# Kernel optimization log

Hardware: AMD Instinct MI355X
Metric: run time of the kernel (lower is better)

The kernel has to match this reference:

```python
import jax, jax.numpy as jnp
import numpy as np

DIM = 1024
D_INNER = 2048

def setup_inputs() -> dict:
    key = jax.random.key(0)
    ks = jax.random.split(key, 8)
    B, T = 8, 1024
    x = jax.random.normal(ks[0], (B, T, DIM), dtype=jnp.float32)
    h0 = jnp.zeros((B, D_INNER), dtype=jnp.float32)
    # params (xavier-ish scales)
    in_proj_w = jax.random.normal(ks[1], (D_INNER, DIM), dtype=jnp.float32) * (2.0 / (DIM + D_INNER)) ** 0.5
    out_proj_w = jax.random.normal(ks[2], (DIM, D_INNER), dtype=jnp.float32) * (2.0 / (DIM + D_INNER)) ** 0.5
    c_h = jax.random.uniform(ks[3], (D_INNER,), jnp.float32, -0.1, 0.1)
    # spectral normalization as in _init_weights
    c_h = c_h * jnp.minimum(1.0, 0.99 / jnp.abs(jnp.fft.fft(c_h)).max())
    c_x = jax.random.uniform(ks[4], (D_INNER,), jnp.float32, -0.1, 0.1)
    c_x = c_x * jnp.minimum(1.0, 0.99 / jnp.abs(jnp.fft.fft(c_x)).max())
    b = jnp.zeros((D_INNER,), dtype=jnp.float32)
    W_gate = jax.random.normal(ks[5], (D_INNER, D_INNER), dtype=jnp.float32) * (1.0 / D_INNER) ** 0.5
    b_gate = jnp.zeros((D_INNER,), dtype=jnp.float32)
    return {"x": x, "h0": h0, "in_proj_w": in_proj_w, "out_proj_w": out_proj_w,
            "c_h": c_h, "c_x": c_x, "b": b, "W_gate": W_gate, "b_gate": b_gate}

def _circ_apply_fft(fft_c, v):
    # circ(c) @ v along last axis via real FFT; v: [..., D]
    D = v.shape[-1]
    return jnp.fft.irfft(fft_c * jnp.fft.rfft(v, axis=-1), n=D, axis=-1)

def reference(x, h0, in_proj_w, out_proj_w, c_h, c_x, b, W_gate, b_gate):
    B, T, _ = x.shape
    D = h0.shape[-1]
    x_proj = jnp.einsum('btd,ed->bte', x, in_proj_w)  # [B,T,D_inner]
    # gate path (fully parallel over T)
    gate = jax.nn.silu(jnp.einsum('bte,fe->btf', x_proj, W_gate) + b_gate)
    # input circulant contribution, parallel over all tokens
    pre = _circ_apply_fft(jnp.fft.rfft(c_x), x_proj) + b  # [B,T,D]
    fft_ch = jnp.fft.rfft(c_h)

    def step(h_prev, pre_t):
        h_new = jnp.tanh(_circ_apply_fft(fft_ch, h_prev) + pre_t)
        return h_new, h_new

    pre_tbd = jnp.transpose(pre, (1, 0, 2))  # [T,B,D]
    h_final, h_seq = jax.lax.scan(step, h0, pre_tbd)  # h_seq: [T,B,D]
    cell_out = jnp.transpose(h_seq, (1, 0, 2)) * gate  # [B,T,D]
    output = jnp.einsum('bte,de->btd', cell_out, out_proj_w)  # [B,T,dim]
    return output, h_final
```

## Files before the change

kernel.cpp:

```cpp
#include <hip/hip_runtime.h>
#include <cstdint>
#include <cstddef>

#define DI 2048
#define DM 1024
#define BB 8
#define TT 1024
#define ROWS (BB*TT)

typedef short  short8 __attribute__((ext_vector_type(8)));
typedef float  f32x4  __attribute__((ext_vector_type(4)));

__device__ __forceinline__ unsigned short f2bf(float f) {
  unsigned int u = __builtin_bit_cast(unsigned int, f);
  u = u + 0x7fffu + ((u >> 16) & 1u);
  return (unsigned short)(u >> 16);
}
__device__ __forceinline__ float fast_tanh(float x) {
  float ax = fabsf(x);
  float e  = __expf(-2.0f * ax);
  float t  = (1.0f - e) / (1.0f + e);
  return x < 0.0f ? -t : t;
}
__device__ __forceinline__ float silu_f(float z) {
  return z / (1.0f + __expf(-z));
}
__device__ __forceinline__ unsigned mulpk(unsigned a, unsigned b) {
  float a0 = __builtin_bit_cast(float, a << 16);
  float a1 = __builtin_bit_cast(float, a & 0xffff0000u);
  float b0 = __builtin_bit_cast(float, b << 16);
  float b1 = __builtin_bit_cast(float, b & 0xffff0000u);
  unsigned r0 = f2bf(a0 * b0), r1 = f2bf(a1 * b1);
  return r0 | (r1 << 16);
}
__device__ __forceinline__ uint4 pack8(const unsigned short* q) {
  uint4 p;
  p.x = (unsigned)q[0] | ((unsigned)q[1] << 16);
  p.y = (unsigned)q[2] | ((unsigned)q[3] << 16);
  p.z = (unsigned)q[4] | ((unsigned)q[5] << 16);
  p.w = (unsigned)q[6] | ((unsigned)q[7] << 16);
  return p;
}

__global__ void cast_k(const float* __restrict__ s, short* __restrict__ d, int n4) {
  int i = blockIdx.x * 256 + threadIdx.x;
  if (i >= n4) return;
  float4 f = ((const float4*)s)[i];
  unsigned lo = (unsigned)f2bf(f.x) | ((unsigned)f2bf(f.y) << 16);
  unsigned hi = (unsigned)f2bf(f.z) | ((unsigned)f2bf(f.w) << 16);
  uint2 o; o.x = lo; o.y = hi;
  ((uint2*)d)[i] = o;
}

__global__ void build_cx_k(const float* __restrict__ cx, short* __restrict__ C) {
  int tid = blockIdx.x * 256 + threadIdx.x;
  int n   = tid >> 8;
  int k0  = (tid & 255) * 8;
  unsigned short q[8];
#pragma unroll
  for (int j = 0; j < 8; ++j) q[j] = f2bf(cx[(n - (k0 + j)) & (DI - 1)]);
  *(uint4*)(C + (size_t)n * DI + k0) = pack8(q);
}

__global__ __launch_bounds__(256) void gemm_k(
    const short* __restrict__ A, const short* __restrict__ A2,
    const short* __restrict__ Bt,
    int M, int N, int K, int mode, const float* __restrict__ bias,
    float* __restrict__ outF, short* __restrict__ outH)
{
  __shared__ __align__(16) short As[128 * 40];
  __shared__ __align__(16) short Bs[128 * 40];
  const int tid  = threadIdx.x;
  const int m0   = blockIdx.y * 128, n0 = blockIdx.x * 128;
  const int wave = tid >> 6, lane = tid & 63;
  const int wy = wave >> 1, wx = wave & 1;
  const int l = lane & 15, G = lane >> 4;
  const int srow = tid >> 1, sseg = tid & 1;

  f32x4 acc[4][4];
#pragma unroll
  for (int i = 0; i < 4; ++i)
#pragma unroll
    for (int j = 0; j < 4; ++j) acc[i][j] = (f32x4){0.f, 0.f, 0.f, 0.f};

  for (int k0 = 0; k0 < K; k0 += 32) {
    if (k0) __syncthreads();
    const short* ga = A  + (size_t)(m0 + srow) * K + k0 + sseg * 16;
    const short* gb = Bt + (size_t)(n0 + srow) * K + k0 + sseg * 16;
    uint4 a0 = *(const uint4*)ga;
    uint4 a1 = *(const uint4*)(ga + 8);
    if (A2) {
      const short* g2 = A2 + (size_t)(m0 + srow) * K + k0 + sseg * 16;
      uint4 m0v = *(const uint4*)g2;
      uint4 m1v = *(const uint4*)(g2 + 8);
      a0.x = mulpk(a0.x, m0v.x); a0.y = mulpk(a0.y, m0v.y);
      a0.z = mulpk(a0.z, m0v.z); a0.w = mulpk(a0.w, m0v.w);
      a1.x = mulpk(a1.x, m1v.x); a1.y = mulpk(a1.y, m1v.y);
      a1.z = mulpk(a1.z, m1v.z); a1.w = mulpk(a1.w, m1v.w);
    }
    uint4 b0 = *(const uint4*)gb;
    uint4 b1 = *(const uint4*)(gb + 8);
    *(uint4*)&As[srow * 40 + sseg * 16]     = a0;
    *(uint4*)&As[srow * 40 + sseg * 16 + 8] = a1;
    *(uint4*)&Bs[srow * 40 + sseg * 16]     = b0;
    *(uint4*)&Bs[srow * 40 + sseg * 16 + 8] = b1;
    __syncthreads();
    short8 af[4], bfv[4];
#pragma unroll
    for (int i = 0; i < 4; ++i) af[i]  = *(const short8*)&As[(64 * wy + 16 * i + l) * 40 + 8 * G];
#pragma unroll
    for (int j = 0; j < 4; ++j) bfv[j] = *(const short8*)&Bs[(64 * wx + 16 * j + l) * 40 + 8 * G];
#pragma unroll
    for (int i = 0; i < 4; ++i)
#pragma unroll
      for (int j = 0; j < 4; ++j)
        acc[i][j] = __builtin_amdgcn_mfma_f32_16x16x32_bf16(af[i], bfv[j], acc[i][j], 0, 0, 0);
  }

#pragma unroll
  for (int j = 0; j < 4; ++j) {
    const int c = n0 + 64 * wx + 16 * j + l;
    float bv = 0.f;
    if (mode == 1 || mode == 2) bv = bias[c];
#pragma unroll
    for (int i = 0; i < 4; ++i) {
      const int r0 = m0 + 64 * wy + 16 * i + 4 * G;
#pragma unroll
      for (int v = 0; v < 4; ++v) {
        float z = acc[i][j][v] + bv;
        size_t off = (size_t)(r0 + v) * N + c;
        if (mode == 0)      outH[off] = (short)f2bf(z);
        else if (mode == 2) outH[off] = (short)f2bf(silu_f(z));
        else                outF[off] = z;
      }
    }
  }
}

__global__ __launch_bounds__(512, 2) void fused_k(
    const float* __restrict__ pre, const float* __restrict__ h0,
    const float* __restrict__ ch, short* __restrict__ hseq,
    float* __restrict__ hfin,
    const short* __restrict__ xproj, const short* __restrict__ wg,
    const float* __restrict__ bg, short* __restrict__ gate)
{
  __shared__ __align__(16) char smem[69632];
  const int bid = blockIdx.x;
  const int tid = threadIdx.x;

  if (bid < BB) {
    short* h_lds = (short*)smem;
    float* part  = (float*)(smem + 4096);
    const int b    = bid;
    const int kg   = tid >> 6;
    const int lane = tid & 63;
    const int q    = lane & 15;
    const int G    = lane >> 4;
    const float* preB = pre + (size_t)b * TT * DI;

    short8 av[22];
#pragma unroll
    for (int idx = 0; idx < 22; ++idx) {
      const int base = 16 * (idx - 14) + q - 8 * G - 256 * kg;
      short8 v;
#pragma unroll
      for (int j = 0; j < 8; ++j)
        v[j] = (short)f2bf(ch[(base - j) & (DI - 1)]);
      av[idx] = v;
    }

    {
      float4 hv = *(const float4*)(h0 + b * DI + 4 * tid);
      unsigned lo = (unsigned)f2bf(hv.x) | ((unsigned)f2bf(hv.y) << 16);
      unsigned hi = (unsigned)f2bf(hv.z) | ((unsigned)f2bf(hv.w) << 16);
      const int blk = tid >> 1;
      const int pb  = blk ^ ((blk >> 4) & 7);
      uint2 w; w.x = lo; w.y = hi;
      *(uint2*)&h_lds[pb * 8 + 4 * (tid & 1)] = w;
    }
    float4 pcur = *(const float4*)(preB + 4 * tid);
    __syncthreads();

    const int rbase = 32 * kg + G + 16 * q;

    for (int t = 0; t < TT; ++t) {
      const float* pn = preB + (size_t)(t + 1 < TT ? t + 1 : t) * DI;
      float4 pf = *(const float4*)(pn + 4 * tid);

      f32x4 acc[8];
#pragma unroll
      for (int mt = 0; mt < 8; ++mt) acc[mt] = (f32x4){0.f, 0.f, 0.f, 0.f};

#pragma unroll
      for (int s = 0; s < 8; ++s) {
        const int blk = (rbase + 4 * s) & 255;
        const int pb  = blk ^ ((blk >> 4) & 7);
        short8 bv = *(const short8*)&h_lds[pb * 8];
#pragma unroll
        for (int mt = 0; mt < 8; ++mt)
          acc[mt] = __builtin_amdgcn_mfma_f32_16x16x32_bf16(av[mt - 2 * s + 14], bv, acc[mt], 0, 0, 0);
      }

      {
        float* pk = part + (kg << 11);
#pragma unroll
        for (int mt = 0; mt < 8; ++mt) {
          const int nb  = 4 * mt + G + 32 * q;
          const int pnb = nb ^ ((nb >> 5) & 7);
          *(f32x4*)&pk[4 * pnb] = acc[mt];
        }
      }
      __syncthreads();

      {
        const int pnb = tid ^ ((tid >> 5) & 7);
        const float* pp = part + 4 * pnb;
        float4 c0 = *(const float4*)(pp);
        float4 c1 = *(const float4*)(pp + 2048);
        float4 c2 = *(const float4*)(pp + 4096);
        float4 c3 = *(const float4*)(pp + 6144);
        float4 c4 = *(const float4*)(pp + 8192);
        float4 c5 = *(const float4*)(pp + 10240);
        float4 c6 = *(const float4*)(pp + 12288);
        float4 c7 = *(const float4*)(pp + 14336);
        float z0 = ((c0.x + c1.x) + (c2.x + c3.x)) + ((c4.x + c5.x) + (c6.x + c7.x)) + pcur.x;
        float z1 = ((c0.y + c1.y) + (c2.y + c3.y)) + ((c4.y + c5.y) + (c6.y + c7.y)) + pcur.y;
        float z2 = ((c0.z + c1.z) + (c2.z + c3.z)) + ((c4.z + c5.z) + (c6.z + c7.z)) + pcur.z;
        float z3 = ((c0.w + c1.w) + (c2.w + c3.w)) + ((c4.w + c5.w) + (c6.w + c7.w)) + pcur.w;
        float t0 = fast_tanh(z0), t1 = fast_tanh(z1);
        float t2 = fast_tanh(z2), t3 = fast_tanh(z3);
        unsigned lo = (unsigned)f2bf(t0) | ((unsigned)f2bf(t1) << 16);
        unsigned hi = (unsigned)f2bf(t2) | ((unsigned)f2bf(t3) << 16);
        const int blk = tid >> 1;
        const int pb  = blk ^ ((blk >> 4) & 7);
        uint2 w; w.x = lo; w.y = hi;
        *(uint2*)&h_lds[pb * 8 + 4 * (tid & 1)] = w;
        *(uint2*)(hseq + (size_t)(b * TT + t) * DI + 4 * tid) = w;
        if (t == TT - 1) {
          float4 hf; hf.x = t0; hf.y = t1; hf.z = t2; hf.w = t3;
          *(float4*)(hfin + b * DI + 4 * tid) = hf;
        }
      }
      __syncthreads();
      pcur = pf;
    }
  } else {
    short* As = (short*)smem;
    short* Bs = (short*)(smem + 20480);
    const int wid = tid >> 6, lane = tid & 63;
    const int wy = wid >> 1, wx = wid & 1;
    const int l = lane & 15, G = lane >> 4;

    for (int tile = bid - BB; tile < 512; tile += 248) {
      const int m0 = (tile & 31) * 256, n0 = (tile >> 5) * 128;
      f32x4 acc[4][4];
#pragma unroll
      for (int i = 0; i < 4; ++i)
#pragma unroll
        for (int j = 0; j < 4; ++j) acc[i][j] = (f32x4){0.f, 0.f, 0.f, 0.f};

      for (int k0 = 0; k0 < DI; k0 += 32) {
        __syncthreads();
        const short* ga = xproj + (size_t)(m0 + (tid >> 1)) * DI + k0 + (tid & 1) * 16;
        const short* gb = wg    + (size_t)(n0 + (tid >> 2)) * DI + k0 + (tid & 3) * 8;
        uint4 a0 = *(const uint4*)ga;
        uint4 a1 = *(const uint4*)(ga + 8);
        uint4 b0 = *(const uint4*)gb;
        *(uint4*)&As[(tid >> 1) * 40 + (tid & 1) * 16]     = a0;
        *(uint4*)&As[(tid >> 1) * 40 + (tid & 1) * 16 + 8] = a1;
        *(uint4*)&Bs[(tid >> 2) * 40 + (tid & 3) * 8]      = b0;
        __syncthreads();
        short8 af[4], bfv[4];
#pragma unroll
        for (int i = 0; i < 4; ++i) af[i]  = *(const short8*)&As[(64 * wy + 16 * i + l) * 40 + 8 * G];
#pragma unroll
        for (int j = 0; j < 4; ++j) bfv[j] = *(const short8*)&Bs[(64 * wx + 16 * j + l) * 40 + 8 * G];
#pragma unroll
        for (int i = 0; i < 4; ++i)
#pragma unroll
          for (int j = 0; j < 4; ++j)
            acc[i][j] = __builtin_amdgcn_mfma_f32_16x16x32_bf16(af[i], bfv[j], acc[i][j], 0, 0, 0);
      }
#pragma unroll
      for (int j = 0; j < 4; ++j) {
        const int c = n0 + 64 * wx + 16 * j + l;
        const float bv = bg[c];
#pragma unroll
        for (int i = 0; i < 4; ++i) {
          const int r0 = m0 + 64 * wy + 16 * i + 4 * G;
#pragma unroll
          for (int v = 0; v < 4; ++v) {
            float z = acc[i][j][v] + bv;
            gate[(size_t)(r0 + v) * DI + c] = (short)f2bf(silu_f(z));
          }
        }
      }
      __syncthreads();
    }
  }
}

extern "C" void kernel_launch(void* const* d_in, const int* in_sizes, int n_in,
                              void* d_out, int out_size, void* d_ws, size_t ws_size,
                              hipStream_t stream) {
  const float* x    = (const float*)d_in[0];
  const float* h0   = (const float*)d_in[1];
  const float* win  = (const float*)d_in[2];
  const float* wout = (const float*)d_in[3];
  const float* ch   = (const float*)d_in[4];
  const float* cx   = (const float*)d_in[5];
  const float* bb   = (const float*)d_in[6];
  const float* wg   = (const float*)d_in[7];
  const float* bg   = (const float*)d_in[8];
  float* out = (float*)d_out;

  char* ws = (char*)d_ws;
  short* o_xb    = (short*)(ws + 0);
  short* o_win   = (short*)(ws + 16777216);
  short* o_cx    = (short*)(ws + 20971520);
  short* o_hseq  = (short*)(ws + 0);
  short* o_xproj = (short*)(ws + 33554432);
  float* o_pre   = (float*)(ws + 67108864);
  short* o_wout  = (short*)(ws + 67108864);
  short* o_gate  = (short*)(ws + 134217728);
  short* o_wg    = (short*)(ws + 167772160);

  cast_k<<<8192, 256, 0, stream>>>(x,   o_xb,  (BB * TT * DM) / 4);
  cast_k<<<2048, 256, 0, stream>>>(win, o_win, (DI * DM) / 4);
  cast_k<<<4096, 256, 0, stream>>>(wg,  o_wg,  (DI * DI) / 4);
  build_cx_k<<<2048, 256, 0, stream>>>(cx, o_cx);

  gemm_k<<<dim3(DI / 128, ROWS / 128), 256, 0, stream>>>(
      o_xb, nullptr, o_win, ROWS, DI, DM, 0, nullptr, nullptr, o_xproj);

  gemm_k<<<dim3(DI / 128, ROWS / 128), 256, 0, stream>>>(
      o_xproj, nullptr, o_cx, ROWS, DI, DI, 1, bb, o_pre, nullptr);

  fused_k<<<256, 512, 0, stream>>>(o_pre, h0, ch, o_hseq,
                                   out + (size_t)BB * TT * DM,
                                   o_xproj, o_wg, bg, o_gate);

  cast_k<<<2048, 256, 0, stream>>>(wout, o_wout, (DM * DI) / 4);

  gemm_k<<<dim3(DM / 128, ROWS / 128), 256, 0, stream>>>(
      o_hseq, o_gate, o_wout, ROWS, DM, DI, 3, nullptr, out, nullptr);
}
```

Baseline: 2.290 ms.

## Process two batch rows per scan block and defer hseq stores

Each scan workgroup now runs two independent batch recurrences, so only four blocks do the scan instead of eight and more blocks are free for the gate GEMM. Interleaving two independent MFMA chains per timestep is meant to hide latency within the serial step and share the circulant register fragments. The hseq global store is deferred by one step to move it off the critical path. In exchange, shared memory doubles to 136KB, which may lower occupancy for the GEMM blocks, and each scan step does twice the work, which can lengthen the serial critical path.

```diff
diff --git a/kernel.cpp b/kernel.cpp
--- a/kernel.cpp
+++ b/kernel.cpp
@@ -7,6 +7,7 @@
 #define BB 8
 #define TT 1024
 #define ROWS (BB*TT)
+#define NSCAN 4
 
 typedef short  short8 __attribute__((ext_vector_type(8)));
 typedef float  f32x4  __attribute__((ext_vector_type(4)));
@@ -144,19 +145,16 @@
     const short* __restrict__ xproj, const short* __restrict__ wg,
     const float* __restrict__ bg, short* __restrict__ gate)
 {
-  __shared__ __align__(16) char smem[69632];
+  __shared__ __align__(16) char smem[139264];
   const int bid = blockIdx.x;
   const int tid = threadIdx.x;
 
-  if (bid < BB) {
-    short* h_lds = (short*)smem;
-    float* part  = (float*)(smem + 4096);
-    const int b    = bid;
+  if (bid < NSCAN) {
+    float* part = (float*)(smem + 8192);
     const int kg   = tid >> 6;
     const int lane = tid & 63;
     const int q    = lane & 15;
     const int G    = lane >> 4;
-    const float* preB = pre + (size_t)b * TT * DI;
 
     short8 av[22];
 #pragma unroll
@@ -169,7 +167,11 @@
       av[idx] = v;
     }
 
-    {
+    float4 pcur[2];
+#pragma unroll
+    for (int bt = 0; bt < 2; ++bt) {
+      short* h_lds = (short*)(smem + bt * 4096);
+      const int b = 2 * bid + bt;
       float4 hv = *(const float4*)(h0 + b * DI + 4 * tid);
       unsigned lo = (unsigned)f2bf(hv.x) | ((unsigned)f2bf(hv.y) << 16);
       unsigned hi = (unsigned)f2bf(hv.z) | ((unsigned)f2bf(hv.w) << 16);
@@ -177,32 +179,44 @@
       const int pb  = blk ^ ((blk >> 4) & 7);
       uint2 w; w.x = lo; w.y = hi;
       *(uint2*)&h_lds[pb * 8 + 4 * (tid & 1)] = w;
-    }
-    float4 pcur = *(const float4*)(preB + 4 * tid);
+      pcur[bt] = *(const float4*)(pre + (size_t)b * TT * DI + 4 * tid);
+    }
     __syncthreads();
 
     const int rbase = 32 * kg + G + 16 * q;
+    uint2 wprev[2];
+    wprev[0] = (uint2){0u, 0u}; wprev[1] = (uint2){0u, 0u};
 
     for (int t = 0; t < TT; ++t) {
-      const float* pn = preB + (size_t)(t + 1 < TT ? t + 1 : t) * DI;
-      float4 pf = *(const float4*)(pn + 4 * tid);
-
-      f32x4 acc[8];
-#pragma unroll
-      for (int mt = 0; mt < 8; ++mt) acc[mt] = (f32x4){0.f, 0.f, 0.f, 0.f};
-
-#pragma unroll
-      for (int s = 0; s < 8; ++s) {
-        const int blk = (rbase + 4 * s) & 255;
-        const int pb  = blk ^ ((blk >> 4) & 7);
-        short8 bv = *(const short8*)&h_lds[pb * 8];
-#pragma unroll
-        for (int mt = 0; mt < 8; ++mt)
-          acc[mt] = __builtin_amdgcn_mfma_f32_16x16x32_bf16(av[mt - 2 * s + 14], bv, acc[mt], 0, 0, 0);
-      }
-
-      {
-        float* pk = part + (kg << 11);
+      float4 pf[2];
+#pragma unroll
+      for (int bt = 0; bt < 2; ++bt) {
+        const float* pn = pre + (size_t)(2 * bid + bt) * TT * DI
+                        + (size_t)(t + 1 < TT ? t + 1 : t) * DI;
+        pf[bt] = *(const float4*)(pn + 4 * tid);
+      }
+      if (t) {
+#pragma unroll
+        for (int bt = 0; bt < 2; ++bt)
+          *(uint2*)(hseq + (size_t)((2 * bid + bt) * TT + t - 1) * DI + 4 * tid) = wprev[bt];
+      }
+
+#pragma unroll
+      for (int bt = 0; bt < 2; ++bt) {
+        const short* h_lds = (const short*)(smem + bt * 4096);
+        f32x4 acc[8];
+#pragma unroll
+        for (int mt = 0; mt < 8; ++mt) acc[mt] = (f32x4){0.f, 0.f, 0.f, 0.f};
+#pragma unroll
+        for (int s = 0; s < 8; ++s) {
+          const int blk = (rbase + 4 * s) & 255;
+          const int pb  = blk ^ ((blk >> 4) & 7);
+          short8 bv = *(const short8*)&h_lds[pb * 8];
+#pragma unroll
+          for (int mt = 0; mt < 8; ++mt)
+            acc[mt] = __builtin_amdgcn_mfma_f32_16x16x32_bf16(av[mt - 2 * s + 14], bv, acc[mt], 0, 0, 0);
+        }
+        float* pk = part + bt * 16384 + (kg << 11);
 #pragma unroll
         for (int mt = 0; mt < 8; ++mt) {
           const int nb  = 4 * mt + G + 32 * q;
@@ -212,9 +226,10 @@
       }
       __syncthreads();
 
-      {
+#pragma unroll
+      for (int bt = 0; bt < 2; ++bt) {
         const int pnb = tid ^ ((tid >> 5) & 7);
-        const float* pp = part + 4 * pnb;
+        const float* pp = part + bt * 16384 + 4 * pnb;
         float4 c0 = *(const float4*)(pp);
         float4 c1 = *(const float4*)(pp + 2048);
         float4 c2 = *(const float4*)(pp + 4096);
@@ -223,10 +238,10 @@
         float4 c5 = *(const float4*)(pp + 10240);
         float4 c6 = *(const float4*)(pp + 12288);
         float4 c7 = *(const float4*)(pp + 14336);
-        float z0 = ((c0.x + c1.x) + (c2.x + c3.x)) + ((c4.x + c5.x) + (c6.x + c7.x)) + pcur.x;
-        float z1 = ((c0.y + c1.y) + (c2.y + c3.y)) + ((c4.y + c5.y) + (c6.y + c7.y)) + pcur.y;
-        float z2 = ((c0.z + c1.z) + (c2.z + c3.z)) + ((c4.z + c5.z) + (c6.z + c7.z)) + pcur.z;
-        float z3 = ((c0.w + c1.w) + (c2.w + c3.w)) + ((c4.w + c5.w) + (c6.w + c7.w)) + pcur.w;
+        float z0 = ((c0.x + c1.x) + (c2.x + c3.x)) + ((c4.x + c5.x) + (c6.x + c7.x)) + pcur[bt].x;
+        float z1 = ((c0.y + c1.y) + (c2.y + c3.y)) + ((c4.y + c5.y) + (c6.y + c7.y)) + pcur[bt].y;
+        float z2 = ((c0.z + c1.z) + (c2.z + c3.z)) + ((c4.z + c5.z) + (c6.z + c7.z)) + pcur[bt].z;
+        float z3 = ((c0.w + c1.w) + (c2.w + c3.w)) + ((c4.w + c5.w) + (c6.w + c7.w)) + pcur[bt].w;
         float t0 = fast_tanh(z0), t1 = fast_tanh(z1);
         float t2 = fast_tanh(z2), t3 = fast_tanh(z3);
         unsigned lo = (unsigned)f2bf(t0) | ((unsigned)f2bf(t1) << 16);
@@ -234,16 +249,20 @@
         const int blk = tid >> 1;
         const int pb  = blk ^ ((blk >> 4) & 7);
         uint2 w; w.x = lo; w.y = hi;
+        short* h_lds = (short*)(smem + bt * 4096);
         *(uint2*)&h_lds[pb * 8 + 4 * (tid & 1)] = w;
-        *(uint2*)(hseq + (size_t)(b * TT + t) * DI + 4 * tid) = w;
+        wprev[bt] = w;
         if (t == TT - 1) {
           float4 hf; hf.x = t0; hf.y = t1; hf.z = t2; hf.w = t3;
-          *(float4*)(hfin + b * DI + 4 * tid) = hf;
+          *(float4*)(hfin + (2 * bid + bt) * DI + 4 * tid) = hf;
         }
       }
       __syncthreads();
-      pcur = pf;
-    }
+      pcur[0] = pf[0]; pcur[1] = pf[1];
+    }
+#pragma unroll
+    for (int bt = 0; bt < 2; ++bt)
+      *(uint2*)(hseq + (size_t)((2 * bid + bt) * TT + TT - 1) * DI + 4 * tid) = wprev[bt];
   } else {
     short* As = (short*)smem;
     short* Bs = (short*)(smem + 20480);
@@ -251,7 +270,7 @@
     const int wy = wid >> 1, wx = wid & 1;
     const int l = lane & 15, G = lane >> 4;
 
-    for (int tile = bid - BB; tile < 512; tile += 248) {
+    for (int tile = bid - NSCAN; tile < 512; tile += (256 - NSCAN)) {
       const int m0 = (tile & 31) * 256, n0 = (tile >> 5) * 128;
       f32x4 acc[4][4];
 #pragma unroll
```

After: 3.780 ms. 1.65x slower.

## Use 32x32x16 MFMA with 4 scan waves and defer hseq stores

Applied to the files above, without the earlier changes.

The recurrent scan step now runs its circulant matvec on only four waves, each using 32x32x16 bf16 MFMAs with two accumulators instead of eight waves of 16x16x32 MFMAs. This halves the cross-wave partial-sum reduction through LDS from eight to four partials. The global store of each hidden state is deferred by one step so it sits off the critical path before the barrier. The cost is more registers per active wave for the circulant fragments, four idle waves during the MFMA phase, and a larger shared allocation that may reduce occupancy for the overlapped gate GEMM blocks.

```diff
diff --git a/kernel.cpp b/kernel.cpp
--- a/kernel.cpp
+++ b/kernel.cpp
@@ -7,9 +7,11 @@
 #define BB 8
 #define TT 1024
 #define ROWS (BB*TT)
+#define NSCAN 8
 
 typedef short  short8 __attribute__((ext_vector_type(8)));
 typedef float  f32x4  __attribute__((ext_vector_type(4)));
+typedef float  f32x16 __attribute__((ext_vector_type(16)));
 
 __device__ __forceinline__ unsigned short f2bf(float f) {
   unsigned int u = __builtin_bit_cast(unsigned int, f);
@@ -144,29 +146,32 @@
     const short* __restrict__ xproj, const short* __restrict__ wg,
     const float* __restrict__ bg, short* __restrict__ gate)
 {
-  __shared__ __align__(16) char smem[69632];
+  __shared__ __align__(16) char smem[81920];
   const int bid = blockIdx.x;
   const int tid = threadIdx.x;
 
-  if (bid < BB) {
+  if (bid < NSCAN) {
     short* h_lds = (short*)smem;
     float* part  = (float*)(smem + 4096);
     const int b    = bid;
-    const int kg   = tid >> 6;
+    const int wid  = tid >> 6;
     const int lane = tid & 63;
-    const int q    = lane & 15;
-    const int G    = lane >> 4;
+    const int kg   = wid;
+    const int qc   = lane & 31;
+    const int Gc   = lane >> 5;
     const float* preB = pre + (size_t)b * TT * DI;
 
-    short8 av[22];
-#pragma unroll
-    for (int idx = 0; idx < 22; ++idx) {
-      const int base = 16 * (idx - 14) + q - 8 * G - 256 * kg;
-      short8 v;
-#pragma unroll
-      for (int j = 0; j < 8; ++j)
-        v[j] = (short)f2bf(ch[(base - j) & (DI - 1)]);
-      av[idx] = v;
+    short8 av[34];
+    if (wid < 4) {
+#pragma unroll
+      for (int idx = 0; idx < 34; ++idx) {
+        const int base = 16 * (idx - 31) + qc - 8 * Gc - 512 * kg;
+        short8 v;
+#pragma unroll
+        for (int j = 0; j < 8; ++j)
+          v[j] = (short)f2bf(ch[(base - j) & (DI - 1)]);
+        av[idx] = v;
+      }
     }
 
     {
@@ -181,52 +186,60 @@
     float4 pcur = *(const float4*)(preB + 4 * tid);
     __syncthreads();
 
-    const int rbase = 32 * kg + G + 16 * q;
+    uint2 wprev; wprev.x = 0u; wprev.y = 0u;
 
     for (int t = 0; t < TT; ++t) {
       const float* pn = preB + (size_t)(t + 1 < TT ? t + 1 : t) * DI;
       float4 pf = *(const float4*)(pn + 4 * tid);
-
-      f32x4 acc[8];
-#pragma unroll
-      for (int mt = 0; mt < 8; ++mt) acc[mt] = (f32x4){0.f, 0.f, 0.f, 0.f};
-
-#pragma unroll
-      for (int s = 0; s < 8; ++s) {
-        const int blk = (rbase + 4 * s) & 255;
-        const int pb  = blk ^ ((blk >> 4) & 7);
-        short8 bv = *(const short8*)&h_lds[pb * 8];
-#pragma unroll
-        for (int mt = 0; mt < 8; ++mt)
-          acc[mt] = __builtin_amdgcn_mfma_f32_16x16x32_bf16(av[mt - 2 * s + 14], bv, acc[mt], 0, 0, 0);
-      }
+      if (t)
+        *(uint2*)(hseq + (size_t)(b * TT + t - 1) * DI + 4 * tid) = wprev;
+
+      if (wid < 4) {
+        f32x16 acc0, acc1;
+#pragma unroll
+        for (int v = 0; v < 16; ++v) { acc0[v] = 0.f; acc1[v] = 0.f; }
+#pragma unroll
+        for (int s = 0; s < 32; ++s) {
+          const int blk = (64 * kg + 2 * s + Gc + 8 * qc) & 255;
+          const int pb  = blk ^ ((blk >> 4) & 7);
+          short8 bv = *(const short8*)&h_lds[pb * 8];
+          acc0 = __builtin_amdgcn_mfma_f32_32x32x16_bf16(av[31 - s], bv, acc0, 0, 0, 0);
+          acc1 = __builtin_amdgcn_mfma_f32_32x32x16_bf16(av[33 - s], bv, acc1, 0, 0, 0);
+        }
+        float* pk = part + (kg << 11);
+#pragma unroll
+        for (int s4 = 0; s4 < 4; ++s4) {
+          {
+            const int nb  = 2 * s4 + Gc + 16 * qc;
+            const int pnb = nb ^ ((nb >> 4) & 7);
+            float4 w;
+            w.x = acc0[4 * s4 + 0]; w.y = acc0[4 * s4 + 1];
+            w.z = acc0[4 * s4 + 2]; w.w = acc0[4 * s4 + 3];
+            *(float4*)&pk[4 * pnb] = w;
+          }
+          {
+            const int nb  = 8 + 2 * s4 + Gc + 16 * qc;
+            const int pnb = nb ^ ((nb >> 4) & 7);
+            float4 w;
+            w.x = acc1[4 * s4 + 0]; w.y = acc1[4 * s4 + 1];
+            w.z = acc1[4 * s4 + 2]; w.w = acc1[4 * s4 + 3];
+            *(float4*)&pk[4 * pnb] = w;
+          }
+        }
+      }
+      __syncthreads();
 
       {
-        float* pk = part + (kg << 11);
-#pragma unroll
-        for (int mt = 0; mt < 8; ++mt) {
-          const int nb  = 4 * mt + G + 32 * q;
-          const int pnb = nb ^ ((nb >> 5) & 7);
-          *(f32x4*)&pk[4 * pnb] = acc[mt];
-        }
-      }
-      __syncthreads();
-
-      {
-        const int pnb = tid ^ ((tid >> 5) & 7);
-        const float* pp = part + 4 * pnb;
+        const int pe = tid ^ ((tid >> 4) & 7);
+        const float* pp = part + 4 * pe;
         float4 c0 = *(const float4*)(pp);
         float4 c1 = *(const float4*)(pp + 2048);
         float4 c2 = *(const float4*)(pp + 4096);
         float4 c3 = *(const float4*)(pp + 6144);
-        float4 c4 = *(const float4*)(pp + 8192);
-        float4 c5 = *(const float4*)(pp + 10240);
-        float4 c6 = *(const float4*)(pp + 12288);
-        float4 c7 = *(const float4*)(pp + 14336);
-        float z0 = ((c0.x + c1.x) + (c2.x + c3.x)) + ((c4.x + c5.x) + (c6.x + c7.x)) + pcur.x;
-        float z1 = ((c0.y + c1.y) + (c2.y + c3.y)) + ((c4.y + c5.y) + (c6.y + c7.y)) + pcur.y;
-        float z2 = ((c0.z + c1.z) + (c2.z + c3.z)) + ((c4.z + c5.z) + (c6.z + c7.z)) + pcur.z;
-        float z3 = ((c0.w + c1.w) + (c2.w + c3.w)) + ((c4.w + c5.w) + (c6.w + c7.w)) + pcur.w;
+        float z0 = (c0.x + c1.x) + (c2.x + c3.x) + pcur.x;
+        float z1 = (c0.y + c1.y) + (c2.y + c3.y) + pcur.y;
+        float z2 = (c0.z + c1.z) + (c2.z + c3.z) + pcur.z;
+        float z3 = (c0.w + c1.w) + (c2.w + c3.w) + pcur.w;
         float t0 = fast_tanh(z0), t1 = fast_tanh(z1);
         float t2 = fast_tanh(z2), t3 = fast_tanh(z3);
         unsigned lo = (unsigned)f2bf(t0) | ((unsigned)f2bf(t1) << 16);
@@ -235,7 +248,7 @@
         const int pb  = blk ^ ((blk >> 4) & 7);
         uint2 w; w.x = lo; w.y = hi;
         *(uint2*)&h_lds[pb * 8 + 4 * (tid & 1)] = w;
-        *(uint2*)(hseq + (size_t)(b * TT + t) * DI + 4 * tid) = w;
+        wprev = w;
         if (t == TT - 1) {
           float4 hf; hf.x = t0; hf.y = t1; hf.z = t2; hf.w = t3;
           *(float4*)(hfin + b * DI + 4 * tid) = hf;
@@ -244,6 +257,7 @@
       __syncthreads();
       pcur = pf;
     }
+    *(uint2*)(hseq + (size_t)(b * TT + TT - 1) * DI + 4 * tid) = wprev;
   } else {
     short* As = (short*)smem;
     short* Bs = (short*)(smem + 20480);
@@ -251,7 +265,7 @@
     const int wy = wid >> 1, wx = wid & 1;
     const int l = lane & 15, G = lane >> 4;
 
-    for (int tile = bid - BB; tile < 512; tile += 248) {
+    for (int tile = bid - NSCAN; tile < 512; tile += (256 - NSCAN)) {
       const int m0 = (tile & 31) * 256, n0 = (tile >> 5) * 128;
       f32x4 acc[4][4];
 #pragma unroll
```

Result: no change. 2.278 ms (-0.5%).

## Split each batch's recurrence across four workgroups synchronized via global flags

Applied to the files above, without the earlier changes.

The serial scan for each batch element now runs on four cooperating workgroups instead of one. Each workgroup computes 512 of the 2048 output channels per step. The workgroups exchange the new hidden state through global memory (hseq) and spin on per-block step counters kept in a scratch region of the output buffer, which is zeroed first. This cuts the MFMA and reduction work per workgroup on the latency-bound critical path, at the cost of a cross-workgroup global-memory handshake every timestep and relaxed-ordering visibility risks. Four fewer... rather, 24 fewer workgroups are left for the concurrent gate GEMM.

```diff
diff --git a/kernel.cpp b/kernel.cpp
--- a/kernel.cpp
+++ b/kernel.cpp
@@ -7,6 +7,7 @@
 #define BB 8
 #define TT 1024
 #define ROWS (BB*TT)
+#define NSCAN 32
 
 typedef short  short8 __attribute__((ext_vector_type(8)));
 typedef float  f32x4  __attribute__((ext_vector_type(4)));
@@ -142,26 +143,26 @@
     const float* __restrict__ ch, short* __restrict__ hseq,
     float* __restrict__ hfin,
     const short* __restrict__ xproj, const short* __restrict__ wg,
-    const float* __restrict__ bg, short* __restrict__ gate)
+    const float* __restrict__ bg, short* __restrict__ gate,
+    unsigned* __restrict__ flags)
 {
-  __shared__ __align__(16) char smem[69632];
+  __shared__ __align__(16) char smem[86016];
   const int bid = blockIdx.x;
   const int tid = threadIdx.x;
 
-  if (bid < BB) {
+  if (bid < NSCAN) {
     short* h_lds = (short*)smem;
     float* part  = (float*)(smem + 4096);
-    const int b    = bid;
-    const int kg   = tid >> 6;
-    const int lane = tid & 63;
-    const int q    = lane & 15;
-    const int G    = lane >> 4;
-    const float* preB = pre + (size_t)b * TT * DI;
-
-    short8 av[22];
-#pragma unroll
-    for (int idx = 0; idx < 22; ++idx) {
-      const int base = 16 * (idx - 14) + q - 8 * G - 256 * kg;
+    const int b = bid >> 2, c = bid & 3;
+    const int w = tid >> 6, lane = tid & 63;
+    const int q = lane & 15, G = lane >> 4;
+    const float* preB = pre + (size_t)b * TT * DI + 512 * c;
+    unsigned* myflag = flags + (4 * b + c) * 32;
+
+    short8 av[16];
+#pragma unroll
+    for (int idx = 0; idx < 16; ++idx) {
+      const int base = 16 * (idx - 14) + q - 8 * G - 256 * w;
       short8 v;
 #pragma unroll
       for (int j = 0; j < 8; ++j)
@@ -175,73 +176,76 @@
       unsigned hi = (unsigned)f2bf(hv.z) | ((unsigned)f2bf(hv.w) << 16);
       const int blk = tid >> 1;
       const int pb  = blk ^ ((blk >> 4) & 7);
-      uint2 w; w.x = lo; w.y = hi;
-      *(uint2*)&h_lds[pb * 8 + 4 * (tid & 1)] = w;
-    }
-    float4 pcur = *(const float4*)(preB + 4 * tid);
-    __syncthreads();
-
-    const int rbase = 32 * kg + G + 16 * q;
+      uint2 wv; wv.x = lo; wv.y = hi;
+      *(uint2*)&h_lds[pb * 8 + 4 * (tid & 1)] = wv;
+    }
+    float pcur = preB[tid];
+
+    const int bbase = 64 * c + 32 * w + 4 * q + G;
 
     for (int t = 0; t < TT; ++t) {
-      const float* pn = preB + (size_t)(t + 1 < TT ? t + 1 : t) * DI;
-      float4 pf = *(const float4*)(pn + 4 * tid);
-
-      f32x4 acc[8];
-#pragma unroll
-      for (int mt = 0; mt < 8; ++mt) acc[mt] = (f32x4){0.f, 0.f, 0.f, 0.f};
-
+      if (t) {
+        const int pc = (lane < 3) ? (lane + (lane >= c ? 1 : 0)) : 0;
+        const unsigned* fp = flags + (4 * b + pc) * 32;
+        while (true) {
+          unsigned v = __hip_atomic_load(fp, __ATOMIC_RELAXED, __HIP_MEMORY_SCOPE_AGENT);
+          bool ok = (lane < 3) ? (v >= (unsigned)t) : true;
+          if (__all(ok)) break;
+          __builtin_amdgcn_s_sleep(2);
+        }
+        const unsigned* rowU = (const unsigned*)(hseq + (size_t)(b * TT + t - 1) * DI);
+        unsigned d0 = __hip_atomic_load(rowU + tid,       __ATOMIC_RELAXED, __HIP_MEMORY_SCOPE_AGENT);
+        unsigned d1 = __hip_atomic_load(rowU + tid + 512, __ATOMIC_RELAXED, __HIP_MEMORY_SCOPE_AGENT);
+        const int blkA = tid >> 2,        pbA = blkA ^ ((blkA >> 4) & 7);
+        const int blkB = (tid + 512) >> 2, pbB = blkB ^ ((blkB >> 4) & 7);
+        *(unsigned*)&h_lds[pbA * 8 + 2 * (tid & 3)] = d0;
+        *(unsigned*)&h_lds[pbB * 8 + 2 * (tid & 3)] = d1;
+      }
+      __syncthreads();
+
+      float pf = preB[(size_t)(t + 1 < TT ? t + 1 : t) * DI + tid];
+
+      f32x4 acc0 = (f32x4){0.f, 0.f, 0.f, 0.f};
+      f32x4 acc1 = (f32x4){0.f, 0.f, 0.f, 0.f};
 #pragma unroll
       for (int s = 0; s < 8; ++s) {
-        const int blk = (rbase + 4 * s) & 255;
+        const int blk = (bbase + 4 * s) & 255;
         const int pb  = blk ^ ((blk >> 4) & 7);
         short8 bv = *(const short8*)&h_lds[pb * 8];
-#pragma unroll
-        for (int mt = 0; mt < 8; ++mt)
-          acc[mt] = __builtin_amdgcn_mfma_f32_16x16x32_bf16(av[mt - 2 * s + 14], bv, acc[mt], 0, 0, 0);
-      }
-
+        acc0 = __builtin_amdgcn_mfma_f32_16x16x32_bf16(av[14 - 2 * s], bv, acc0, 0, 0, 0);
+        acc1 = __builtin_amdgcn_mfma_f32_16x16x32_bf16(av[15 - 2 * s], bv, acc1, 0, 0, 0);
+      }
       {
-        float* pk = part + (kg << 11);
-#pragma unroll
-        for (int mt = 0; mt < 8; ++mt) {
-          const int nb  = 4 * mt + G + 32 * q;
-          const int pnb = nb ^ ((nb >> 5) & 7);
-          *(f32x4*)&pk[4 * pnb] = acc[mt];
+        float* pk = part + (w << 9);
+        const int f0 = 8 * q + G,     p0 = f0 ^ ((f0 >> 4) & 7);
+        const int f1 = 8 * q + 4 + G, p1 = f1 ^ ((f1 >> 4) & 7);
+        *(f32x4*)&pk[4 * p0] = acc0;
+        *(f32x4*)&pk[4 * p1] = acc1;
+      }
+      __syncthreads();
+
+      {
+        const int f = tid >> 2, vv = tid & 3;
+        const int pfz = f ^ ((f >> 4) & 7);
+        const int off = 4 * pfz + vv;
+        float z = ((part[off] + part[512 + off]) + (part[1024 + off] + part[1536 + off]))
+                + ((part[2048 + off] + part[2560 + off]) + (part[3072 + off] + part[3584 + off]))
+                + pcur;
+        float th = fast_tanh(z);
+        unsigned hv = (unsigned)f2bf(th);
+        unsigned other = (unsigned)__shfl_xor((int)hv, 1);
+        if (!(lane & 1)) {
+          unsigned dw = (hv & 0xffffu) | (other << 16);
+          unsigned* rowO = (unsigned*)(hseq + (size_t)(b * TT + t) * DI);
+          __hip_atomic_store(rowO + 256 * c + (tid >> 1), dw,
+                             __ATOMIC_RELAXED, __HIP_MEMORY_SCOPE_AGENT);
         }
+        if (t == TT - 1) hfin[b * DI + 512 * c + tid] = th;
       }
       __syncthreads();
-
-      {
-        const int pnb = tid ^ ((tid >> 5) & 7);
-        const float* pp = part + 4 * pnb;
-        float4 c0 = *(const float4*)(pp);
-        float4 c1 = *(const float4*)(pp + 2048);
-        float4 c2 = *(const float4*)(pp + 4096);
-        float4 c3 = *(const float4*)(pp + 6144);
-        float4 c4 = *(const float4*)(pp + 8192);
-        float4 c5 = *(const float4*)(pp + 10240);
-        float4 c6 = *(const float4*)(pp + 12288);
-        float4 c7 = *(const float4*)(pp + 14336);
-        float z0 = ((c0.x + c1.x) + (c2.x + c3.x)) + ((c4.x + c5.x) + (c6.x + c7.x)) + pcur.x;
-        float z1 = ((c0.y + c1.y) + (c2.y + c3.y)) + ((c4.y + c5.y) + (c6.y + c7.y)) + pcur.y;
-        float z2 = ((c0.z + c1.z) + (c2.z + c3.z)) + ((c4.z + c5.z) + (c6.z + c7.z)) + pcur.z;
-        float z3 = ((c0.w + c1.w) + (c2.w + c3.w)) + ((c4.w + c5.w) + (c6.w + c7.w)) + pcur.w;
-        float t0 = fast_tanh(z0), t1 = fast_tanh(z1);
-        float t2 = fast_tanh(z2), t3 = fast_tanh(z3);
-        unsigned lo = (unsigned)f2bf(t0) | ((unsigned)f2bf(t1) << 16);
-        unsigned hi = (unsigned)f2bf(t2) | ((unsigned)f2bf(t3) << 16);
-        const int blk = tid >> 1;
-        const int pb  = blk ^ ((blk >> 4) & 7);
-        uint2 w; w.x = lo; w.y = hi;
-        *(uint2*)&h_lds[pb * 8 + 4 * (tid & 1)] = w;
-        *(uint2*)(hseq + (size_t)(b * TT + t) * DI + 4 * tid) = w;
-        if (t == TT - 1) {
-          float4 hf; hf.x = t0; hf.y = t1; hf.z = t2; hf.w = t3;
-          *(float4*)(hfin + b * DI + 4 * tid) = hf;
-        }
-      }
-      __syncthreads();
+      if (tid == 0)
+        __hip_atomic_store(myflag, (unsigned)(t + 1),
+                           __ATOMIC_RELAXED, __HIP_MEMORY_SCOPE_AGENT);
       pcur = pf;
     }
   } else {
@@ -251,7 +255,7 @@
     const int wy = wid >> 1, wx = wid & 1;
     const int l = lane & 15, G = lane >> 4;
 
-    for (int tile = bid - BB; tile < 512; tile += 248) {
+    for (int tile = bid - NSCAN; tile < 512; tile += (256 - NSCAN)) {
       const int m0 = (tile & 31) * 256, n0 = (tile >> 5) * 128;
       f32x4 acc[4][4];
 #pragma unroll
@@ -283,15 +287,15 @@
       }
 #pragma unroll
       for (int j = 0; j < 4; ++j) {
-        const int c = n0 + 64 * wx + 16 * j + l;
-        const float bv = bg[c];
+        const int cidx = n0 + 64 * wx + 16 * j + l;
+        const float bv = bg[cidx];
 #pragma unroll
         for (int i = 0; i < 4; ++i) {
           const int r0 = m0 + 64 * wy + 16 * i + 4 * G;
 #pragma unroll
           for (int v = 0; v < 4; ++v) {
             float z = acc[i][j][v] + bv;
-            gate[(size_t)(r0 + v) * DI + c] = (short)f2bf(silu_f(z));
+            gate[(size_t)(r0 + v) * DI + cidx] = (short)f2bf(silu_f(z));
           }
         }
       }
@@ -336,9 +340,12 @@
   gemm_k<<<dim3(DI / 128, ROWS / 128), 256, 0, stream>>>(
       o_xproj, nullptr, o_cx, ROWS, DI, DI, 1, bb, o_pre, nullptr);
 
+  hipMemsetAsync(d_out, 0, 4096, stream);
+
   fused_k<<<256, 512, 0, stream>>>(o_pre, h0, ch, o_hseq,
                                    out + (size_t)BB * TT * DM,
-                                   o_xproj, o_wg, bg, o_gate);
+                                   o_xproj, o_wg, bg, o_gate,
+                                   (unsigned*)d_out);
 
   cast_k<<<2048, 256, 0, stream>>>(wout, o_wout, (DM * DI) / 4);
 
```

After: 2.222 ms. -3.0%, faster.
